# Kernel tuning notes

Hardware: AMD Instinct MI355X
Metric: run time of the kernel (lower is better)

The kernel has to match this reference:

```python
import jax, jax.numpy as jnp
import numpy as np

NEG_SLOPE = 0.05

def _leaky(v):
    return jnp.where(v >= 0, v, NEG_SLOPE * v)

def setup_inputs() -> dict:
    key = jax.random.key(0)
    ks = jax.random.split(key, 9)
    B, N, D = 8, 96, 16
    H0, H1, OUT = 50, 50, 64
    x = jax.random.normal(ks[0], (B, N, D), dtype=jnp.float32)
    # dense 0/1 adjacency (float, used directly in matmuls), avg degree ~ 0.15*N
    adj = (jax.random.uniform(ks[1], (B, N, N)) < 0.15).astype(jnp.float32)
    h1 = 3 * D + 3          # 51
    h2 = 2 * D + H0 + 1     # 83
    h3 = D + H1             # 66
    W1 = jax.random.normal(ks[2], (h1, H0), dtype=jnp.float32) / np.sqrt(h1)
    b1 = jax.random.normal(ks[3], (H0,), dtype=jnp.float32) * 0.01
    W2 = jax.random.normal(ks[4], (h2, H1), dtype=jnp.float32) / np.sqrt(h2)
    b2 = jax.random.normal(ks[5], (H1,), dtype=jnp.float32) * 0.01
    W3 = jax.random.normal(ks[6], (h3, OUT), dtype=jnp.float32) / np.sqrt(h3)
    b3 = jax.random.normal(ks[7], (OUT,), dtype=jnp.float32) * 0.01
    return {"x": x, "adj": adj, "W1": W1, "b1": b1, "W2": W2, "b2": b2, "W3": W3, "b3": b3}

def reference(x, adj, W1, b1, W2, b2, W3, b3):
    # Faithful math of SpatialGraphConv.forward, with the O(N^4)/O(N^3)
    # broadcast+concat+GEMM algebraically decomposed into O(N^2) einsums
    # (identical result: the concat-GEMM is a sum of per-block contributions).
    B, N, D = x.shape
    H0 = W1.shape[1]
    # pairwise distances dis[b,i,j]
    diff = x[:, :, None, :] - x[:, None, :, :]            # (B,N,N,D)
    dis = jnp.sqrt(jnp.sum(diff * diff, axis=-1) + 1e-10)  # (B,N,N)
    # split W1 rows per concat block [x_i | x_j | x_k | d_ij | d_jk | d_ik]
    Wxi, Wxj, Wxk = W1[:D], W1[D:2 * D], W1[2 * D:3 * D]
    w_ij, w_jk, w_ik = W1[3 * D], W1[3 * D + 1], W1[3 * D + 2]  # (H0,)
    A = x @ Wxi   # (B,N,H0), indexed by i
    Bm = x @ Wxj  # (B,N,H0), indexed by j
    C = x @ Wxk   # (B,N,H0), indexed by k
    # m3_sum[b,i,j,h] = adj[b,i,j] * sum_k adj[b,j,k] * m3pre[b,i,j,k,h]
    deg = jnp.sum(adj, axis=-1)                           # (B,N): sum_k adj[b,j,k]
    sumC = jnp.einsum('bjk,bkh->bjh', adj, C)             # (B,N,H0)
    sd_jk = jnp.sum(adj * dis, axis=-1)                   # (B,N): sum_k adj[j,k]*dis[j,k]
    sd_ik = jnp.einsum('bik,bjk->bij', dis, adj)          # (B,N,N): sum_k adj[j,k]*dis[i,k]
    S = (deg[:, None, :, None] * (A[:, :, None, :] + Bm[:, None, :, :] + b1
                                   + dis[..., None] * w_ij)
         + sumC[:, None, :, :]
         + sd_jk[:, None, :, None] * w_jk
         + sd_ik[..., None] * w_ik)                        # (B,N,N,H0)
    m3_sum = _leaky(adj[..., None] * S)                    # (B,N,N,H0)
    # stage 2: pairwise concat [x_i | x_j | dis | m3_sum] -> MLP -> adj-masked sum over j
    xi = jnp.broadcast_to(x[:, :, None, :], (B, N, N, D))
    xj = jnp.broadcast_to(x[:, None, :, :], (B, N, N, D))
    feat2 = jnp.concatenate([xi, xj, dis[..., None], m3_sum], axis=-1)  # (B,N,N,2D+1+H0)
    m2 = feat2 @ W2 + b2                                   # (B,N,N,H1)
    m2_sum = _leaky(jnp.einsum('bijh,bij->bih', m2, adj))  # (B,N,H1)
    # stage 3: node-wise MLP
    m1 = _leaky(jnp.concatenate([x, m2_sum], axis=-1) @ W3 + b3)  # (B,N,OUT)
    return m1
```

## Files before the change

kernel.cpp:

```cpp
#include <hip/hip_runtime.h>
#include <math.h>

#define BB   8
#define NN   96
#define DD   16
#define H0D  50
#define H1D  50
#define OUTD 64
#define XP   17

typedef unsigned long long u64;


__global__ __launch_bounds__(256) void sgc_one(
    const float* __restrict__ x, const float* __restrict__ adj,
    const float* __restrict__ W1, const float* __restrict__ b1,
    const float* __restrict__ W2, const float* __restrict__ b2,
    const float* __restrict__ W3, const float* __restrict__ b3,
    float* __restrict__ out)
{
    const int b = blockIdx.x / NN, i = blockIdx.x % NN;
    const int tid = threadIdx.x, wv = tid >> 6, lane = tid & 63;

    __shared__ float sx[NN * XP];
    __shared__ float sdisI[NN];
    __shared__ int   nbrs[NN];
    __shared__ int   scnt;
    __shared__ u64   smi[2];
    __shared__ float sA[H0D];
    __shared__ float sP[NN * H0D];
    __shared__ float sdegc[NN], ssdjkc[NN], ssdikc[NN];
    __shared__ float pmsum[4 * 64];
    __shared__ float smsum[H0D];
    __shared__ float sm2[H1D];
    __shared__ float snxi[DD];
    __shared__ float sdegi, ssdjki;

    const float4* x4 = (const float4*)(x + (size_t)b * NN * DD);
    for (int t = tid; t < NN * DD / 4; t += 256) {
        float4 v = x4[t];
        int row = t >> 2, d = (t & 3) * 4;
        float* p = &sx[row * XP + d];
        p[0] = v.x; p[1] = v.y; p[2] = v.z; p[3] = v.w;
    }
    if (wv == 0) {
        const float* arow = adj + ((size_t)b * NN + i) * NN;
        u64 m0 = __ballot(arow[lane] != 0.f);
        float a1 = (lane < 32) ? arow[64 + lane] : 0.f;
        u64 m1 = __ballot(a1 != 0.f);
        int c0 = __popcll(m0);
        if ((m0 >> lane) & 1)
            nbrs[__popcll(m0 & ((1ull << lane) - 1))] = lane;
        if (lane < 32 && ((m1 >> lane) & 1))
            nbrs[c0 + __popcll(m1 & ((1ull << lane) - 1))] = 64 + lane;
        if (lane == 0) {
            int c = c0 + __popcll(m1);
            scnt = c;
            smi[0] = m0; smi[1] = m1;
            sdegi = (float)c;
        }
    }
    __syncthreads();

    if (tid < NN) {
        const float* xi = &sx[i * XP];
        const float* xk = &sx[tid * XP];
        float s = 1e-10f;
        #pragma unroll
        for (int d = 0; d < DD; ++d) { float t = xi[d] - xk[d]; s += t * t; }
        sdisI[tid] = sqrtf(s);
    } else if (tid < NN + H0D) {
        int h = tid - NN;
        float s = 0.f;
        #pragma unroll
        for (int d = 0; d < DD; ++d) s += sx[i * XP + d] * W1[d * H0D + h];
        sA[h] = s;
    }
    __syncthreads();

    const int cnt = scnt;
    {
        const int hl = (lane < H0D) ? lane : H0D - 1;
        float wxj[DD], wxk[DD];
        #pragma unroll
        for (int d = 0; d < DD; ++d) {
            wxj[d] = W1[(DD + d) * H0D + hl];
            wxk[d] = W1[(2 * DD + d) * H0D + hl];
        }
        const int ch = lane >> 4, dd = lane & 15;
        for (int c = wv; c < cnt; c += 4) {
            const int j = nbrs[c];
            const float* arow = adj + ((size_t)b * NN + j) * NN;
            u64 mj0 = __ballot(arow[lane] != 0.f);
            float a1 = (lane < 32) ? arow[64 + lane] : 0.f;
            u64 mj1 = __ballot(a1 != 0.f);
            float deg = (float)(__popcll(mj0) + __popcll(mj1));
            const float* xj = &sx[j * XP];
            float d0, d1 = 0.f;
            {
                float s = 1e-10f;
                const float* xk = &sx[lane * XP];
                #pragma unroll
                for (int d = 0; d < DD; ++d) { float t = xj[d] - xk[d]; s += t * t; }
                d0 = sqrtf(s);
            }
            if (lane < 32) {
                float s = 1e-10f;
                const float* xk = &sx[(64 + lane) * XP];
                #pragma unroll
                for (int d = 0; d < DD; ++d) { float t = xj[d] - xk[d]; s += t * t; }
                d1 = sqrtf(s);
            }
            float p1 = ((mj0 >> lane) & 1) ? d0 : 0.f;
            float p2 = ((mj0 >> lane) & 1) ? sdisI[lane] : 0.f;
            if (lane < 32 && ((mj1 >> lane) & 1)) { p1 += d1; p2 += sdisI[64 + lane]; }
            #pragma unroll
            for (int off = 1; off < 64; off <<= 1) {
                p1 += __shfl_xor(p1, off, 64);
                p2 += __shfl_xor(p2, off, 64);
            }
            unsigned sm;
            if (ch == 0)      sm = (unsigned)(mj0 & 0xFFFFFFu);
            else if (ch == 1) sm = (unsigned)((mj0 >> 24) & 0xFFFFFFu);
            else if (ch == 2) sm = (unsigned)((mj0 >> 48) & 0xFFFFu) | ((unsigned)(mj1 & 0xFFu) << 16);
            else              sm = (unsigned)((mj1 >> 8) & 0xFFFFFFu);
            float nxv = 0.f;
            const int base = ch * 24;
            while (sm) {
                int k = base + __ffs(sm) - 1;
                sm &= sm - 1;
                nxv += sx[k * XP + dd];
            }
            nxv += __shfl_xor(nxv, 16, 64);
            nxv += __shfl_xor(nxv, 32, 64);
            float bm = 0.f, sc = 0.f;
            #pragma unroll
            for (int d = 0; d < DD; ++d) {
                bm += xj[d] * wxj[d];
                sc += __shfl(nxv, d, 64) * wxk[d];
            }
            if (lane < H0D) sP[c * H0D + lane] = deg * bm + sc;
            if (lane == 0) { sdegc[c] = deg; ssdjkc[c] = p1; ssdikc[c] = p2; }
        }
        if (wv == 0) {
            u64 mi0 = smi[0], mi1 = smi[1];
            float p = ((mi0 >> lane) & 1) ? sdisI[lane] : 0.f;
            if (lane < 32 && ((mi1 >> lane) & 1)) p += sdisI[64 + lane];
            #pragma unroll
            for (int off = 1; off < 64; off <<= 1) p += __shfl_xor(p, off, 64);
            if (lane == 0) ssdjki = p;
            unsigned sm;
            if (ch == 0)      sm = (unsigned)(mi0 & 0xFFFFFFu);
            else if (ch == 1) sm = (unsigned)((mi0 >> 24) & 0xFFFFFFu);
            else if (ch == 2) sm = (unsigned)((mi0 >> 48) & 0xFFFFu) | ((unsigned)(mi1 & 0xFFu) << 16);
            else              sm = (unsigned)((mi1 >> 8) & 0xFFFFFFu);
            float nxv = 0.f;
            const int base = ch * 24;
            while (sm) {
                int k = base + __ffs(sm) - 1;
                sm &= sm - 1;
                nxv += sx[k * XP + dd];
            }
            nxv += __shfl_xor(nxv, 16, 64);
            nxv += __shfl_xor(nxv, 32, 64);
            if (lane < DD) snxi[lane] = nxv;
        }
    }
    __syncthreads();

    {
        const int hl = (lane < H0D) ? lane : H0D - 1;
        float b1v = b1[hl];
        float wij = W1[(3 * DD + 0) * H0D + hl];
        float wjk = W1[(3 * DD + 1) * H0D + hl];
        float wik = W1[(3 * DD + 2) * H0D + hl];
        float abv = sA[hl] + b1v;
        float msum = 0.f;
        for (int c = wv; c < cnt; c += 4) {
            float S = sdegc[c] * (abv + sdisI[nbrs[c]] * wij)
                    + sP[c * H0D + hl] + ssdjkc[c] * wjk + ssdikc[c] * wik;
            msum += (S >= 0.f) ? S : 0.05f * S;
        }
        pmsum[wv * 64 + lane] = msum;
    }
    __syncthreads();

    if (tid < H0D)
        smsum[tid] = pmsum[tid] + pmsum[64 + tid] + pmsum[128 + tid] + pmsum[192 + tid];
    __syncthreads();

    if (tid < H1D) {
        float dg = sdegi;
        float s = dg * b2[tid];
        #pragma unroll
        for (int d = 0; d < DD; ++d)
            s += dg * sx[i * XP + d] * W2[d * H1D + tid]
               + snxi[d] * W2[(DD + d) * H1D + tid];
        s += ssdjki * W2[(2 * DD) * H1D + tid];
        for (int c = 0; c < H0D; ++c)
            s += smsum[c] * W2[(2 * DD + 1 + c) * H1D + tid];
        sm2[tid] = (s >= 0.f) ? s : 0.05f * s;
    }
    __syncthreads();

    if (tid < OUTD) {
        float s = b3[tid];
        #pragma unroll
        for (int d = 0; d < DD; ++d) s += sx[i * XP + d] * W3[d * OUTD + tid];
        for (int h = 0; h < H1D; ++h) s += sm2[h] * W3[(DD + h) * OUTD + tid];
        s = (s >= 0.f) ? s : 0.05f * s;
        out[((size_t)b * NN + i) * OUTD + tid] = s;
    }
}

extern "C" void kernel_launch(void* const* d_in, const int* in_sizes, int n_in,
                              void* d_out, int out_size, void* d_ws, size_t ws_size,
                              hipStream_t stream) {
    const float* x   = (const float*)d_in[0];
    const float* adj = (const float*)d_in[1];
    const float* W1  = (const float*)d_in[2];
    const float* b1  = (const float*)d_in[3];
    const float* W2  = (const float*)d_in[4];
    const float* b2  = (const float*)d_in[5];
    const float* W3  = (const float*)d_in[6];
    const float* b3  = (const float*)d_in[7];
    float* out = (float*)d_out;

    sgc_one<<<BB * NN, 256, 0, stream>>>(x, adj, W1, b1, W2, b2, W3, b3, out);
}
```

Before: 85.69 us.

## Restructure neighbor stage into chunked block-wide phases with shared W1 and staged adj rows

The neighbor processing moves from one wave per neighbor to chunks of up to 32 neighbors handled block-wide. Each chunk stages its adjacency rows in shared memory, computes only the masked distances instead of all 96 per neighbor, and spreads the P projection over all 256 threads. W1 is cached in shared memory, and W2/W3 are read once into a dummy sum as a cache prefetch. The cost is more barriers per chunk and extra shared-memory traffic. Work also becomes serialised over chunks for high-degree nodes.

```diff
diff --git a/kernel.cpp b/kernel.cpp
--- a/kernel.cpp
+++ b/kernel.cpp
@@ -8,11 +8,12 @@
 #define H1D  50
 #define OUTD 64
 #define XP   17
+#define MAXC 32
 
 typedef unsigned long long u64;
 
 
-__global__ __launch_bounds__(256) void sgc_one(
+__global__ __launch_bounds__(256) void sgc5(
     const float* __restrict__ x, const float* __restrict__ adj,
     const float* __restrict__ W1, const float* __restrict__ b1,
     const float* __restrict__ W2, const float* __restrict__ b2,
@@ -23,42 +24,59 @@
     const int tid = threadIdx.x, wv = tid >> 6, lane = tid & 63;
 
     __shared__ float sx[NN * XP];
+    __shared__ float sW1[51 * H0D];
+    __shared__ float srows[MAXC * NN];
     __shared__ float sdisI[NN];
     __shared__ int   nbrs[NN];
-    __shared__ int   scnt;
+    __shared__ u64   smasks[MAXC][2];
     __shared__ u64   smi[2];
     __shared__ float sA[H0D];
-    __shared__ float sP[NN * H0D];
-    __shared__ float sdegc[NN], ssdjkc[NN], ssdikc[NN];
-    __shared__ float pmsum[4 * 64];
-    __shared__ float smsum[H0D];
-    __shared__ float sm2[H1D];
-    __shared__ float snxi[DD];
-    __shared__ float sdegi, ssdjki;
+    __shared__ float sP[MAXC * H0D];
+    __shared__ float snxc[MAXC * DD];
+    __shared__ float spjk[MAXC * 8], spik[MAXC * 8];
+    __shared__ float sdegc[MAXC], ssdjkc[MAXC], ssdikc[MAXC];
+    __shared__ float smsum[H0D], sm2[H1D], snxi[DD];
+    __shared__ float sdummy[64];
+    __shared__ float ssdjki_s;
+    __shared__ int   scnt;
+
+    float b1v = 0.f, b2v = 0.f, b3v = 0.f;
 
     const float4* x4 = (const float4*)(x + (size_t)b * NN * DD);
     for (int t = tid; t < NN * DD / 4; t += 256) {
         float4 v = x4[t];
-        int row = t >> 2, d = (t & 3) * 4;
-        float* p = &sx[row * XP + d];
+        float* p = &sx[(t >> 2) * XP + (t & 3) * 4];
         p[0] = v.x; p[1] = v.y; p[2] = v.z; p[3] = v.w;
+    }
+    const float2* w12 = (const float2*)W1;
+    for (int t = tid; t < 51 * H0D / 2; t += 256) {
+        float2 v = w12[t];
+        sW1[2 * t] = v.x; sW1[2 * t + 1] = v.y;
     }
     if (wv == 0) {
         const float* arow = adj + ((size_t)b * NN + i) * NN;
-        u64 m0 = __ballot(arow[lane] != 0.f);
+        float a0 = arow[lane];
         float a1 = (lane < 32) ? arow[64 + lane] : 0.f;
+        u64 m0 = __ballot(a0 != 0.f);
         u64 m1 = __ballot(a1 != 0.f);
-        int c0 = __popcll(m0);
+        int c0n = __popcll(m0);
         if ((m0 >> lane) & 1)
             nbrs[__popcll(m0 & ((1ull << lane) - 1))] = lane;
         if (lane < 32 && ((m1 >> lane) & 1))
-            nbrs[c0 + __popcll(m1 & ((1ull << lane) - 1))] = 64 + lane;
-        if (lane == 0) {
-            int c = c0 + __popcll(m1);
-            scnt = c;
-            smi[0] = m0; smi[1] = m1;
-            sdegi = (float)c;
-        }
+            nbrs[c0n + __popcll(m1 & ((1ull << lane) - 1))] = 64 + lane;
+        if (lane == 0) { smi[0] = m0; smi[1] = m1; scnt = c0n + __popcll(m1); }
+    }
+    if (tid < H0D)  b1v = b1[tid];
+    if (tid < H1D)  b2v = b2[tid];
+    if (tid < OUTD) b3v = b3[tid];
+    if (tid < H0D)  smsum[tid] = 0.f;
+    {
+        float ws = 0.f;
+        const float2* w22 = (const float2*)W2;
+        for (int t = tid; t < 83 * H1D / 2; t += 256) { float2 v = w22[t]; ws += v.x + v.y; }
+        const float4* w34 = (const float4*)W3;
+        for (int t = tid; t < 66 * OUTD / 4; t += 256) { float4 v = w34[t]; ws += v.x + v.y + v.z + v.w; }
+        sdummy[lane] = ws;
     }
     __syncthreads();
 
@@ -73,143 +91,158 @@
         int h = tid - NN;
         float s = 0.f;
         #pragma unroll
-        for (int d = 0; d < DD; ++d) s += sx[i * XP + d] * W1[d * H0D + h];
+        for (int d = 0; d < DD; ++d) s += sx[i * XP + d] * sW1[d * H0D + h];
         sA[h] = s;
     }
     __syncthreads();
 
+    if (tid < DD) {
+        u64 m0 = smi[0], m1 = smi[1];
+        float s = 0.f;
+        while (m0) { int k = __ffsll(m0) - 1;      m0 &= m0 - 1; s += sx[k * XP + tid]; }
+        while (m1) { int k = 64 + __ffsll(m1) - 1; m1 &= m1 - 1; s += sx[k * XP + tid]; }
+        snxi[tid] = s;
+    } else if (tid == DD) {
+        u64 m0 = smi[0], m1 = smi[1];
+        float s = 0.f;
+        while (m0) { int k = __ffsll(m0) - 1;      m0 &= m0 - 1; s += sdisI[k]; }
+        while (m1) { int k = 64 + __ffsll(m1) - 1; m1 &= m1 - 1; s += sdisI[k]; }
+        ssdjki_s = s;
+    }
+
     const int cnt = scnt;
-    {
-        const int hl = (lane < H0D) ? lane : H0D - 1;
-        float wxj[DD], wxk[DD];
-        #pragma unroll
-        for (int d = 0; d < DD; ++d) {
-            wxj[d] = W1[(DD + d) * H0D + hl];
-            wxk[d] = W1[(2 * DD + d) * H0D + hl];
-        }
-        const int ch = lane >> 4, dd = lane & 15;
-        for (int c = wv; c < cnt; c += 4) {
-            const int j = nbrs[c];
-            const float* arow = adj + ((size_t)b * NN + j) * NN;
-            u64 mj0 = __ballot(arow[lane] != 0.f);
-            float a1 = (lane < 32) ? arow[64 + lane] : 0.f;
-            u64 mj1 = __ballot(a1 != 0.f);
-            float deg = (float)(__popcll(mj0) + __popcll(mj1));
-            const float* xj = &sx[j * XP];
-            float d0, d1 = 0.f;
-            {
-                float s = 1e-10f;
-                const float* xk = &sx[lane * XP];
+    const float degi = (float)cnt;
+
+    for (int c0 = 0; c0 < cnt; c0 += MAXC) {
+        const int cc = min(MAXC, cnt - c0);
+
+        for (int t = tid; t < cc * 24; t += 256) {
+            int c = t / 24, f = t % 24;
+            const float4 v = *(const float4*)(adj + ((size_t)b * NN + nbrs[c0 + c]) * NN + f * 4);
+            float* p = &srows[c * NN + f * 4];
+            p[0] = v.x; p[1] = v.y; p[2] = v.z; p[3] = v.w;
+        }
+        __syncthreads();
+        for (int c = wv; c < cc; c += 4) {
+            float v0 = srows[c * NN + lane];
+            float v1 = (lane < 32) ? srows[c * NN + 64 + lane] : 0.f;
+            u64 m0 = __ballot(v0 != 0.f);
+            u64 m1 = __ballot(v1 != 0.f);
+            if (lane == 0) {
+                smasks[c][0] = m0; smasks[c][1] = m1;
+                sdegc[c] = (float)(__popcll(m0) + __popcll(m1));
+            }
+        }
+        __syncthreads();
+
+        {
+            int c = tid >> 3, seg = tid & 7;
+            if (c < cc) {
+                u64 m0 = smasks[c][0], m1 = smasks[c][1];
+                int s = seg * 12;
+                u64 wnd;
+                if (s < 64) {
+                    wnd = m0 >> s;
+                    if (s) wnd |= (m1 << (64 - s));
+                } else {
+                    wnd = m1 >> (s - 64);
+                }
+                wnd &= 0xFFFull;
+                const float* xj = &sx[nbrs[c0 + c] * XP];
+                float pjk = 0.f, pik = 0.f;
+                while (wnd) {
+                    int k = s + __ffsll(wnd) - 1;
+                    wnd &= wnd - 1;
+                    const float* xk = &sx[k * XP];
+                    float ss = 1e-10f;
+                    #pragma unroll
+                    for (int d = 0; d < DD; ++d) { float t = xj[d] - xk[d]; ss += t * t; }
+                    pjk += sqrtf(ss);
+                    pik += sdisI[k];
+                }
+                spjk[c * 8 + seg] = pjk;
+                spik[c * 8 + seg] = pik;
+            }
+        }
+        __syncthreads();
+
+        if (tid < 2 * MAXC) {
+            int c = tid >> 1;
+            if (c < cc) {
+                const float* p = (tid & 1) ? &spjk[c * 8] : &spik[c * 8];
+                float s = p[0] + p[1] + p[2] + p[3] + p[4] + p[5] + p[6] + p[7];
+                if (tid & 1) ssdjkc[c] = s; else ssdikc[c] = s;
+            }
+        }
+        for (int u = tid; u < cc * DD; u += 256) {
+            int c = u >> 4, d = u & 15;
+            u64 m0 = smasks[c][0], m1 = smasks[c][1];
+            float s = 0.f;
+            while (m0) { int k = __ffsll(m0) - 1;      m0 &= m0 - 1; s += sx[k * XP + d]; }
+            while (m1) { int k = 64 + __ffsll(m1) - 1; m1 &= m1 - 1; s += sx[k * XP + d]; }
+            snxc[u] = s;
+        }
+        __syncthreads();
+
+        #pragma unroll
+        for (int r = 0; r < 7; ++r) {
+            int u = r * 256 + tid;
+            int c = u / H0D, h = u - c * H0D;
+            if (c < cc) {
+                const float* xj = &sx[nbrs[c0 + c] * XP];
+                const float* nx = &snxc[c * DD];
+                float bm = 0.f, sc = 0.f;
                 #pragma unroll
-                for (int d = 0; d < DD; ++d) { float t = xj[d] - xk[d]; s += t * t; }
-                d0 = sqrtf(s);
-            }
-            if (lane < 32) {
-                float s = 1e-10f;
-                const float* xk = &sx[(64 + lane) * XP];
-                #pragma unroll
-                for (int d = 0; d < DD; ++d) { float t = xj[d] - xk[d]; s += t * t; }
-                d1 = sqrtf(s);
-            }
-            float p1 = ((mj0 >> lane) & 1) ? d0 : 0.f;
-            float p2 = ((mj0 >> lane) & 1) ? sdisI[lane] : 0.f;
-            if (lane < 32 && ((mj1 >> lane) & 1)) { p1 += d1; p2 += sdisI[64 + lane]; }
-            #pragma unroll
-            for (int off = 1; off < 64; off <<= 1) {
-                p1 += __shfl_xor(p1, off, 64);
-                p2 += __shfl_xor(p2, off, 64);
-            }
-            unsigned sm;
-            if (ch == 0)      sm = (unsigned)(mj0 & 0xFFFFFFu);
-            else if (ch == 1) sm = (unsigned)((mj0 >> 24) & 0xFFFFFFu);
-            else if (ch == 2) sm = (unsigned)((mj0 >> 48) & 0xFFFFu) | ((unsigned)(mj1 & 0xFFu) << 16);
-            else              sm = (unsigned)((mj1 >> 8) & 0xFFFFFFu);
-            float nxv = 0.f;
-            const int base = ch * 24;
-            while (sm) {
-                int k = base + __ffs(sm) - 1;
-                sm &= sm - 1;
-                nxv += sx[k * XP + dd];
-            }
-            nxv += __shfl_xor(nxv, 16, 64);
-            nxv += __shfl_xor(nxv, 32, 64);
-            float bm = 0.f, sc = 0.f;
-            #pragma unroll
-            for (int d = 0; d < DD; ++d) {
-                bm += xj[d] * wxj[d];
-                sc += __shfl(nxv, d, 64) * wxk[d];
-            }
-            if (lane < H0D) sP[c * H0D + lane] = deg * bm + sc;
-            if (lane == 0) { sdegc[c] = deg; ssdjkc[c] = p1; ssdikc[c] = p2; }
-        }
-        if (wv == 0) {
-            u64 mi0 = smi[0], mi1 = smi[1];
-            float p = ((mi0 >> lane) & 1) ? sdisI[lane] : 0.f;
-            if (lane < 32 && ((mi1 >> lane) & 1)) p += sdisI[64 + lane];
-            #pragma unroll
-            for (int off = 1; off < 64; off <<= 1) p += __shfl_xor(p, off, 64);
-            if (lane == 0) ssdjki = p;
-            unsigned sm;
-            if (ch == 0)      sm = (unsigned)(mi0 & 0xFFFFFFu);
-            else if (ch == 1) sm = (unsigned)((mi0 >> 24) & 0xFFFFFFu);
-            else if (ch == 2) sm = (unsigned)((mi0 >> 48) & 0xFFFFu) | ((unsigned)(mi1 & 0xFFu) << 16);
-            else              sm = (unsigned)((mi1 >> 8) & 0xFFFFFFu);
-            float nxv = 0.f;
-            const int base = ch * 24;
-            while (sm) {
-                int k = base + __ffs(sm) - 1;
-                sm &= sm - 1;
-                nxv += sx[k * XP + dd];
-            }
-            nxv += __shfl_xor(nxv, 16, 64);
-            nxv += __shfl_xor(nxv, 32, 64);
-            if (lane < DD) snxi[lane] = nxv;
-        }
+                for (int d = 0; d < DD; ++d) {
+                    bm += xj[d] * sW1[(DD + d) * H0D + h];
+                    sc += nx[d] * sW1[(2 * DD + d) * H0D + h];
+                }
+                sP[c * H0D + h] = sdegc[c] * bm + sc;
+            }
+        }
+        __syncthreads();
+
+        if (tid < H0D) {
+            const int h = tid;
+            const float abv = sA[h] + b1v;
+            const float wij = sW1[(3 * DD + 0) * H0D + h];
+            const float wjk = sW1[(3 * DD + 1) * H0D + h];
+            const float wik = sW1[(3 * DD + 2) * H0D + h];
+            float acc = 0.f;
+            for (int c = 0; c < cc; ++c) {
+                float S = sdegc[c] * (abv + sdisI[nbrs[c0 + c]] * wij)
+                        + sP[c * H0D + h] + ssdjkc[c] * wjk + ssdikc[c] * wik;
+                acc += (S >= 0.f) ? S : 0.05f * S;
+            }
+            smsum[h] += acc;
+        }
+        __syncthreads();
+    }
+
+    if (tid < H1D) {
+        const int h = tid;
+        float s = degi * b2v;
+        #pragma unroll
+        for (int d = 0; d < DD; ++d)
+            s += degi * sx[i * XP + d] * W2[d * H1D + h]
+               + snxi[d] * W2[(DD + d) * H1D + h];
+        s += ssdjki_s * W2[(2 * DD) * H1D + h];
+        #pragma unroll
+        for (int c = 0; c < H0D; ++c)
+            s += smsum[c] * W2[(2 * DD + 1 + c) * H1D + h];
+        sm2[h] = (s >= 0.f) ? s : 0.05f * s;
     }
     __syncthreads();
 
-    {
-        const int hl = (lane < H0D) ? lane : H0D - 1;
-        float b1v = b1[hl];
-        float wij = W1[(3 * DD + 0) * H0D + hl];
-        float wjk = W1[(3 * DD + 1) * H0D + hl];
-        float wik = W1[(3 * DD + 2) * H0D + hl];
-        float abv = sA[hl] + b1v;
-        float msum = 0.f;
-        for (int c = wv; c < cnt; c += 4) {
-            float S = sdegc[c] * (abv + sdisI[nbrs[c]] * wij)
-                    + sP[c * H0D + hl] + ssdjkc[c] * wjk + ssdikc[c] * wik;
-            msum += (S >= 0.f) ? S : 0.05f * S;
-        }
-        pmsum[wv * 64 + lane] = msum;
-    }
-    __syncthreads();
-
-    if (tid < H0D)
-        smsum[tid] = pmsum[tid] + pmsum[64 + tid] + pmsum[128 + tid] + pmsum[192 + tid];
-    __syncthreads();
-
-    if (tid < H1D) {
-        float dg = sdegi;
-        float s = dg * b2[tid];
-        #pragma unroll
-        for (int d = 0; d < DD; ++d)
-            s += dg * sx[i * XP + d] * W2[d * H1D + tid]
-               + snxi[d] * W2[(DD + d) * H1D + tid];
-        s += ssdjki * W2[(2 * DD) * H1D + tid];
-        for (int c = 0; c < H0D; ++c)
-            s += smsum[c] * W2[(2 * DD + 1 + c) * H1D + tid];
-        sm2[tid] = (s >= 0.f) ? s : 0.05f * s;
-    }
-    __syncthreads();
-
     if (tid < OUTD) {
-        float s = b3[tid];
-        #pragma unroll
-        for (int d = 0; d < DD; ++d) s += sx[i * XP + d] * W3[d * OUTD + tid];
-        for (int h = 0; h < H1D; ++h) s += sm2[h] * W3[(DD + h) * OUTD + tid];
+        const int o = tid;
+        float s = b3v;
+        #pragma unroll
+        for (int d = 0; d < DD; ++d) s += sx[i * XP + d] * W3[d * OUTD + o];
+        #pragma unroll
+        for (int h = 0; h < H1D; ++h) s += sm2[h] * W3[(DD + h) * OUTD + o];
         s = (s >= 0.f) ? s : 0.05f * s;
-        out[((size_t)b * NN + i) * OUTD + tid] = s;
+        out[((size_t)b * NN + i) * OUTD + o] = s;
     }
 }
 
@@ -226,5 +259,5 @@
     const float* b3  = (const float*)d_in[7];
     float* out = (float*)d_out;
 
-    sgc_one<<<BB * NN, 256, 0, stream>>>(x, adj, W1, b1, W2, b2, W3, b3, out);
+    sgc5<<<BB * NN, 256, 0, stream>>>(x, adj, W1, b1, W2, b2, W3, b3, out);
 }
```

After: 95.64 us. +11.6%, slower.
